# Performance work log

Measured on AMD Instinct MI355X. Metric: run time of the kernel, lower is better.

## Reference

```python
import jax, jax.numpy as jnp
import numpy as np


def setup_inputs() -> dict:
    key = jax.random.key(0)
    k1, k2, k3, k4, k5 = jax.random.split(key, 5)
    B, S, H, K = 64, 2048, 512, 1024  # batch, src_len, hidden, key_size=2*hidden
    return {
        "query": jax.random.normal(k1, (B, 1, H), dtype=jnp.float32),
        "proj_key": jax.random.normal(k2, (B, S, H), dtype=jnp.float32),
        "encoder_hidden": jax.random.normal(k3, (B, S, K), dtype=jnp.float32),
        "mask": jnp.ones((B, 1, S), dtype=jnp.int32),
        "W_q": jax.random.normal(k4, (H, H), dtype=jnp.float32) * (1.0 / np.sqrt(H)),
        "v_energy": jax.random.normal(k5, (H,), dtype=jnp.float32) * (1.0 / np.sqrt(H)),
    }


def reference(query, proj_key, encoder_hidden, mask, W_q, v_energy):
    # query_layer: [B,1,H] @ W_q^T -> [B,1,H]
    q = jnp.einsum("bqe,he->bqh", query, W_q)
    # energy_layer(tanh(q + proj_key)): broadcast add over S, dot with v -> [B,S]
    scores = jnp.einsum("bsh,h->bs", jnp.tanh(q + proj_key), v_energy)
    scores = scores[:, None, :]  # [B,1,S]  (squeeze(2).unsqueeze(1))
    scores = jnp.where(mask == 0, -jnp.inf, scores)
    alphas = jax.nn.softmax(scores, axis=-1)  # [B,1,S]
    context = jnp.einsum("bqs,bsk->bqk", alphas, encoder_hidden)  # [B,1,K]
    return context, alphas
```

## Files before the change

### kernel.cpp

```cpp
#include <hip/hip_runtime.h>
#include <math.h>

#define BB 64
#define SS 2048
#define HH 512
#define KK 1024

__device__ __forceinline__ float fast_tanh(float x) {
    float e = __expf(2.0f * x);
    return 1.0f - 2.0f / (e + 1.0f);
}

__global__ __launch_bounds__(256) void qproj_kernel(
        const float* __restrict__ query,
        const float* __restrict__ Wq,
        float* __restrict__ q_out) {
    int wave = threadIdx.x >> 6;
    int lane = threadIdx.x & 63;
    int o = blockIdx.x * 4 + wave;
    int b = o >> 9;
    int h = o & (HH - 1);
    const float4* wrow = (const float4*)(Wq + (size_t)h * HH);
    const float4* qrow = (const float4*)(query + (size_t)b * HH);
    float4 w0 = wrow[lane * 2 + 0];
    float4 w1 = wrow[lane * 2 + 1];
    float4 x0 = qrow[lane * 2 + 0];
    float4 x1 = qrow[lane * 2 + 1];
    float acc = w0.x * x0.x + w0.y * x0.y + w0.z * x0.z + w0.w * x0.w
              + w1.x * x1.x + w1.y * x1.y + w1.z * x1.z + w1.w * x1.w;
    #pragma unroll
    for (int off = 32; off > 0; off >>= 1)
        acc += __shfl_down(acc, off, 64);
    if (lane == 0) q_out[o] = acc;
}

__global__ __launch_bounds__(256) void score_kernel(
        const float* __restrict__ pk,
        const float* __restrict__ q,
        const float* __restrict__ v,
        float* __restrict__ scores) {
    int wave = threadIdx.x >> 6;
    int lane = threadIdx.x & 63;
    int r = blockIdx.x * 4 + wave;
    int b = r >> 11;
    const float4* prow = (const float4*)(pk + (size_t)r * HH);
    const float4* qrow = (const float4*)(q + (size_t)b * HH);
    const float4* vrow = (const float4*)v;
    float acc = 0.0f;
    #pragma unroll
    for (int i = 0; i < 2; ++i) {
        float4 p = prow[lane * 2 + i];
        float4 qq = qrow[lane * 2 + i];
        float4 vv = vrow[lane * 2 + i];
        acc += fast_tanh(qq.x + p.x) * vv.x;
        acc += fast_tanh(qq.y + p.y) * vv.y;
        acc += fast_tanh(qq.z + p.z) * vv.z;
        acc += fast_tanh(qq.w + p.w) * vv.w;
    }
    #pragma unroll
    for (int off = 32; off > 0; off >>= 1)
        acc += __shfl_down(acc, off, 64);
    if (lane == 0) scores[r] = acc;
}

__global__ __launch_bounds__(256) void softmax_kernel(
        float* __restrict__ alphas,
        const int* __restrict__ mask) {
    int b = blockIdx.x;
    int t = threadIdx.x;
    float* row = alphas + (size_t)b * SS;
    const int* mrow = mask + (size_t)b * SS;
    int base = t * 8;

    float4 s0 = *(const float4*)(row + base);
    float4 s1 = *(const float4*)(row + base + 4);
    int4  m0 = *(const int4*)(mrow + base);
    int4  m1 = *(const int4*)(mrow + base + 4);
    float v[8];
    v[0] = m0.x ? s0.x : -INFINITY;
    v[1] = m0.y ? s0.y : -INFINITY;
    v[2] = m0.z ? s0.z : -INFINITY;
    v[3] = m0.w ? s0.w : -INFINITY;
    v[4] = m1.x ? s1.x : -INFINITY;
    v[5] = m1.y ? s1.y : -INFINITY;
    v[6] = m1.z ? s1.z : -INFINITY;
    v[7] = m1.w ? s1.w : -INFINITY;

    __shared__ float redmax[4];
    __shared__ float redsum[4];
    __shared__ float smax, ssum;

    float mx = v[0];
    #pragma unroll
    for (int i = 1; i < 8; ++i) mx = fmaxf(mx, v[i]);
    #pragma unroll
    for (int off = 32; off > 0; off >>= 1)
        mx = fmaxf(mx, __shfl_xor(mx, off, 64));
    if ((t & 63) == 0) redmax[t >> 6] = mx;
    __syncthreads();
    if (t == 0) smax = fmaxf(fmaxf(redmax[0], redmax[1]), fmaxf(redmax[2], redmax[3]));
    __syncthreads();
    mx = smax;

    float e[8];
    float sum = 0.0f;
    #pragma unroll
    for (int i = 0; i < 8; ++i) { e[i] = __expf(v[i] - mx); sum += e[i]; }
    #pragma unroll
    for (int off = 32; off > 0; off >>= 1)
        sum += __shfl_xor(sum, off, 64);
    if ((t & 63) == 0) redsum[t >> 6] = sum;
    __syncthreads();
    if (t == 0) ssum = redsum[0] + redsum[1] + redsum[2] + redsum[3];
    __syncthreads();
    float inv = 1.0f / ssum;

    float4 o0 = make_float4(e[0] * inv, e[1] * inv, e[2] * inv, e[3] * inv);
    float4 o1 = make_float4(e[4] * inv, e[5] * inv, e[6] * inv, e[7] * inv);
    *(float4*)(row + base)     = o0;
    *(float4*)(row + base + 4) = o1;
}

__global__ __launch_bounds__(256) void zero_kernel(float* __restrict__ p, int n) {
    int i = blockIdx.x * 256 + threadIdx.x;
    if (i < n) p[i] = 0.0f;
}

#define SCHUNK 128
__global__ __launch_bounds__(256) void context_kernel(
        const float* __restrict__ eh,
        const float* __restrict__ alphas,
        float* __restrict__ ctx) {
    int chunk = blockIdx.x;
    int b = blockIdx.y;
    int t = threadIdx.x;
    __shared__ float a_sm[SCHUNK];
    if (t < SCHUNK) a_sm[t] = alphas[(size_t)b * SS + chunk * SCHUNK + t];
    __syncthreads();
    const float4* base = (const float4*)(eh + ((size_t)b * SS + (size_t)chunk * SCHUNK) * KK);
    float4 acc = make_float4(0.f, 0.f, 0.f, 0.f);
    #pragma unroll 4
    for (int s = 0; s < SCHUNK; ++s) {
        float a = a_sm[s];
        float4 x = base[(size_t)s * (KK / 4) + t];
        acc.x += a * x.x;
        acc.y += a * x.y;
        acc.z += a * x.z;
        acc.w += a * x.w;
    }
    float* c = ctx + (size_t)b * KK + t * 4;
    atomicAdd(c + 0, acc.x);
    atomicAdd(c + 1, acc.y);
    atomicAdd(c + 2, acc.z);
    atomicAdd(c + 3, acc.w);
}

extern "C" void kernel_launch(void* const* d_in, const int* in_sizes, int n_in,
                              void* d_out, int out_size, void* d_ws, size_t ws_size,
                              hipStream_t stream) {
    const float* query    = (const float*)d_in[0];
    const float* proj_key = (const float*)d_in[1];
    const float* eh       = (const float*)d_in[2];
    const int*   mask     = (const int*)  d_in[3];
    const float* Wq       = (const float*)d_in[4];
    const float* venergy  = (const float*)d_in[5];

    float* ctx    = (float*)d_out;
    float* alphas = (float*)d_out + BB * KK;

    float* q_tmp = ctx;

    qproj_kernel<<<(BB * HH) / 4, 256, 0, stream>>>(query, Wq, q_tmp);

    score_kernel<<<(BB * SS) / 4, 256, 0, stream>>>(proj_key, q_tmp, venergy, alphas);

    softmax_kernel<<<BB, 256, 0, stream>>>(alphas, mask);

    zero_kernel<<<(BB * KK) / 256, 256, 0, stream>>>(ctx, BB * KK);

    context_kernel<<<dim3(SS / SCHUNK, BB), 256, 0, stream>>>(eh, alphas, ctx);
}
```

Baseline: 828.9 us.

## Replace atomic context accumulation with partial buffers plus reduce kernel

The context computation now uses 32 chunks of 64 source positions per batch instead of 16 chunks of 128. Each block writes its float4 partial sums to a workspace buffer, and a separate reduce kernel sums them, which removes the zero kernel and the float atomics. The qproj and score kernels also switch to lane-contiguous float4 indexing so loads coalesce. In exchange, partials take extra workspace and add an extra write and read of 8 MB.

```diff
diff --git a/kernel.cpp b/kernel.cpp
--- a/kernel.cpp
+++ b/kernel.cpp
@@ -5,6 +5,9 @@
 #define SS 2048
 #define HH 512
 #define KK 1024
+
+#define NCHUNK 32
+#define SCH (SS / NCHUNK)
 
 __device__ __forceinline__ float fast_tanh(float x) {
     float e = __expf(2.0f * x);
@@ -22,12 +25,13 @@
     int h = o & (HH - 1);
     const float4* wrow = (const float4*)(Wq + (size_t)h * HH);
     const float4* qrow = (const float4*)(query + (size_t)b * HH);
-    float4 w0 = wrow[lane * 2 + 0];
-    float4 w1 = wrow[lane * 2 + 1];
-    float4 x0 = qrow[lane * 2 + 0];
-    float4 x1 = qrow[lane * 2 + 1];
-    float acc = w0.x * x0.x + w0.y * x0.y + w0.z * x0.z + w0.w * x0.w
-              + w1.x * x1.x + w1.y * x1.y + w1.z * x1.z + w1.w * x1.w;
+    float acc = 0.0f;
+    #pragma unroll
+    for (int i = 0; i < 2; ++i) {
+        float4 w = wrow[i * 64 + lane];
+        float4 x = qrow[i * 64 + lane];
+        acc += w.x * x.x + w.y * x.y + w.z * x.z + w.w * x.w;
+    }
     #pragma unroll
     for (int off = 32; off > 0; off >>= 1)
         acc += __shfl_down(acc, off, 64);
@@ -49,9 +53,9 @@
     float acc = 0.0f;
     #pragma unroll
     for (int i = 0; i < 2; ++i) {
-        float4 p = prow[lane * 2 + i];
-        float4 qq = qrow[lane * 2 + i];
-        float4 vv = vrow[lane * 2 + i];
+        float4 p  = prow[i * 64 + lane];
+        float4 qq = qrow[i * 64 + lane];
+        float4 vv = vrow[i * 64 + lane];
         acc += fast_tanh(qq.x + p.x) * vv.x;
         acc += fast_tanh(qq.y + p.y) * vv.y;
         acc += fast_tanh(qq.z + p.z) * vv.z;
@@ -121,26 +125,20 @@
     *(float4*)(row + base + 4) = o1;
 }
 
-__global__ __launch_bounds__(256) void zero_kernel(float* __restrict__ p, int n) {
-    int i = blockIdx.x * 256 + threadIdx.x;
-    if (i < n) p[i] = 0.0f;
-}
-
-#define SCHUNK 128
-__global__ __launch_bounds__(256) void context_kernel(
+__global__ __launch_bounds__(256) void ctx_partial_kernel(
         const float* __restrict__ eh,
         const float* __restrict__ alphas,
-        float* __restrict__ ctx) {
+        float* __restrict__ partial) {
     int chunk = blockIdx.x;
     int b = blockIdx.y;
     int t = threadIdx.x;
-    __shared__ float a_sm[SCHUNK];
-    if (t < SCHUNK) a_sm[t] = alphas[(size_t)b * SS + chunk * SCHUNK + t];
+    __shared__ float a_sm[SCH];
+    if (t < SCH) a_sm[t] = alphas[(size_t)b * SS + chunk * SCH + t];
     __syncthreads();
-    const float4* base = (const float4*)(eh + ((size_t)b * SS + (size_t)chunk * SCHUNK) * KK);
+    const float4* base = (const float4*)(eh + ((size_t)b * SS + (size_t)chunk * SCH) * KK);
     float4 acc = make_float4(0.f, 0.f, 0.f, 0.f);
-    #pragma unroll 4
-    for (int s = 0; s < SCHUNK; ++s) {
+    #pragma unroll 8
+    for (int s = 0; s < SCH; ++s) {
         float a = a_sm[s];
         float4 x = base[(size_t)s * (KK / 4) + t];
         acc.x += a * x.x;
@@ -148,11 +146,23 @@
         acc.z += a * x.z;
         acc.w += a * x.w;
     }
-    float* c = ctx + (size_t)b * KK + t * 4;
-    atomicAdd(c + 0, acc.x);
-    atomicAdd(c + 1, acc.y);
-    atomicAdd(c + 2, acc.z);
-    atomicAdd(c + 3, acc.w);
+    ((float4*)partial)[((size_t)chunk * BB + b) * (KK / 4) + t] = acc;
+}
+
+__global__ __launch_bounds__(64) void ctx_reduce_kernel(
+        const float* __restrict__ partial,
+        float* __restrict__ ctx) {
+    int b = blockIdx.x;
+    int kq = blockIdx.y;
+    int t = threadIdx.x;
+    int ki = kq * 64 + t;
+    float4 acc = make_float4(0.f, 0.f, 0.f, 0.f);
+    #pragma unroll
+    for (int c = 0; c < NCHUNK; ++c) {
+        float4 x = ((const float4*)partial)[((size_t)c * BB + b) * (KK / 4) + ki];
+        acc.x += x.x; acc.y += x.y; acc.z += x.z; acc.w += x.w;
+    }
+    ((float4*)ctx)[(size_t)b * (KK / 4) + ki] = acc;
 }
 
 extern "C" void kernel_launch(void* const* d_in, const int* in_sizes, int n_in,
@@ -168,7 +178,8 @@
     float* ctx    = (float*)d_out;
     float* alphas = (float*)d_out + BB * KK;
 
-    float* q_tmp = ctx;
+    float* partial = (float*)d_ws;
+    float* q_tmp   = (float*)d_ws + NCHUNK * BB * KK;
 
     qproj_kernel<<<(BB * HH) / 4, 256, 0, stream>>>(query, Wq, q_tmp);
 
@@ -176,7 +187,7 @@
 
     softmax_kernel<<<BB, 256, 0, stream>>>(alphas, mask);
 
-    zero_kernel<<<(BB * KK) / 256, 256, 0, stream>>>(ctx, BB * KK);
+    ctx_partial_kernel<<<dim3(NCHUNK, BB), 256, 0, stream>>>(eh, alphas, partial);
 
-    context_kernel<<<dim3(SS / SCHUNK, BB), 256, 0, stream>>>(eh, alphas, ctx);
+    ctx_reduce_kernel<<<dim3(BB, 4), 64, 0, stream>>>(partial, ctx);
 }
```

Result: no change. 834.1 us (+0.6%).
